# Optimization experiments

Measured on AMD Instinct MI355X. Metric: run time of the kernel, lower is better.

The kernel has to match this reference:

```python
import jax, jax.numpy as jnp
import numpy as np

N, E, C0, H, NC = 50000, 800000, 64, 64, 2500
NUM_LAYERS = 3


def setup_inputs() -> dict:
    key = jax.random.key(0)
    ks = jax.random.split(key, 16)
    inp = {}
    inp["x"] = jax.random.normal(ks[0], (N, C0), dtype=jnp.float32)
    inp["edge_index"] = jax.random.randint(ks[1], (2, E), 0, N, dtype=jnp.int64)
    inp["cluster"] = jax.random.randint(ks[2], (N,), 0, NC, dtype=jnp.int64)
    c = C0
    for i in range(NUM_LAYERS):
        inp[f"w1_{i}"] = jax.random.normal(ks[3 + 4 * i], (c, H), jnp.float32) / np.sqrt(c).astype(np.float32)
        inp[f"b1_{i}"] = jnp.zeros((H,), jnp.float32)
        inp[f"w2_{i}"] = jax.random.normal(ks[4 + 4 * i], (H, c), jnp.float32) / np.sqrt(H).astype(np.float32)
        inp[f"b2_{i}"] = jnp.zeros((c,), jnp.float32)
        c *= 2
    inp["n_clusters"] = NC
    return inp


def _glp(x, src, dst, w1, b1, w2, b2, num_nodes):
    # node encoder MLP: Linear -> ReLU -> Linear
    h = jnp.maximum(x @ w1 + b1, 0.0) @ w2 + b2  # [N, c]
    # message passing: gather at source, scatter-max at destination
    msg = h[src]  # [E, c]
    aggr = jax.ops.segment_max(msg, dst, num_segments=num_nodes)  # [N, c]
    # nodes with no incoming edges -> 0 (PyG fill for max aggregation)
    aggr = jnp.where(jnp.isfinite(aggr), aggr, 0.0)
    # update: concat(encoder_out, aggregated) -> channels double
    return jnp.concatenate([h, aggr], axis=1)


def reference(x, edge_index, cluster,
              w1_0, b1_0, w2_0, b2_0,
              w1_1, b1_1, w2_1, b2_1,
              w1_2, b1_2, w2_2, b2_2,
              n_clusters):
    num_nodes = x.shape[0]
    src, dst = edge_index[0], edge_index[1]
    params = [(w1_0, b1_0, w2_0, b2_0), (w1_1, b1_1, w2_1, b2_1), (w1_2, b1_2, w2_2, b2_2)]
    for (w1, b1, w2, b2) in params:
        x = _glp(x, src, dst, w1, b1, w2, b2, num_nodes)
    # cluster-wise max pool over polylines
    pooled = jax.ops.segment_max(x, cluster, num_segments=n_clusters)  # [NC, 512]
    pooled = jnp.where(jnp.isfinite(pooled), pooled, 0.0)
    # column-wise (dim=0) normalization as in the source
    out = pooled / (jnp.linalg.norm(pooled, axis=0) + 1e-6)
    return out
```

## Files before the change

### kernel.cpp

```cpp
#include <hip/hip_runtime.h>
#include <math.h>

typedef unsigned short bfu;
typedef __attribute__((ext_vector_type(8))) short bf16x8;
typedef __attribute__((ext_vector_type(16))) float f32x16;

__device__ __forceinline__ float b2f(bfu u) {
    unsigned int x = ((unsigned int)u) << 16;
    return __uint_as_float(x);
}
__device__ __forceinline__ bfu f2bf(float f) {
    unsigned int u = __float_as_uint(f);
    unsigned int r = (u + 0x7FFFu + ((u >> 16) & 1u)) >> 16;
    return (bfu)r;
}

struct InitArgs {
    int* deg; int N; int* cdeg; int NC; float* sumsq;
    const float* w[6]; bfu* whi[6]; bfu* wlo[6]; int K[6]; int Nw[6];
    const float* x0; bfu* xhi; bfu* xlo; int xtotal;
};

__global__ __launch_bounds__(256) void k_init(InitArgs a) {
    const int j = blockIdx.y;
    const int g0 = blockIdx.x * 256 + threadIdx.x;
    const int gs = gridDim.x * 256;
    if (j == 0) {
        for (int i = g0; i < a.N; i += gs) a.deg[i] = 0;
        for (int i = g0; i < a.NC; i += gs) a.cdeg[i] = 0;
        for (int i = g0; i < 512; i += gs) a.sumsq[i] = 0.f;
    } else if (j <= 6) {
        const int jj = j - 1;
        const int K = a.K[jj], Nw = a.Nw[jj];
        const int total = K * Nw;
        const float* w = a.w[jj];
        bfu* dhi = a.whi[jj];
        bfu* dlo = a.wlo[jj];
        for (int idx = g0; idx < total; idx += gs) {
            int k = idx / Nw, n = idx % Nw;
            float v = w[idx];
            bfu hi = f2bf(v);
            bfu lo = f2bf(v - b2f(hi));
            dhi[n * K + k] = hi;
            dlo[n * K + k] = lo;
        }
    } else {
        for (int i = g0; i * 4 < a.xtotal; i += gs) {
            int base = i * 4;
            float4 v = *(const float4*)&a.x0[base];
            ushort4 h, l;
            h.x = f2bf(v.x); l.x = f2bf(v.x - b2f(h.x));
            h.y = f2bf(v.y); l.y = f2bf(v.y - b2f(h.y));
            h.z = f2bf(v.z); l.z = f2bf(v.z - b2f(h.z));
            h.w = f2bf(v.w); l.w = f2bf(v.w - b2f(h.w));
            *(ushort4*)&a.xhi[base] = h;
            *(ushort4*)&a.xlo[base] = l;
        }
    }
}

__global__ void k_rank(const int* __restrict__ dst, int E, int* __restrict__ deg,
                       int* __restrict__ rank,
                       const int* __restrict__ cluster, int N, int* __restrict__ cdeg,
                       int* __restrict__ crank) {
    const int base = blockIdx.x * 1024 + threadIdx.x;
#pragma unroll
    for (int u = 0; u < 4; u++) {
        int e = base + u * 256;
        if (e < E) rank[e] = atomicAdd(&deg[dst[e]], 1);
    }
#pragma unroll
    for (int u = 0; u < 4; u++) {
        int i = base + u * 256;
        if (i < N) crank[i] = atomicAdd(&cdeg[cluster[i]], 1);
    }
}

__global__ __launch_bounds__(256) void k_scanA(const int* __restrict__ deg, int N,
                                               const int* __restrict__ cdeg, int NC,
                                               int* __restrict__ scn0, int* __restrict__ scn1,
                                               int* __restrict__ bsum0, int* __restrict__ bsum1) {
    __shared__ int part[256];
    const int seg = blockIdx.y;
    const int n = seg ? NC : N;
    const int* d = seg ? cdeg : deg;
    int* scn = seg ? scn1 : scn0;
    int* bs  = seg ? bsum1 : bsum0;
    const int b = blockIdx.x;
    if (b * 256 >= n) return;
    const int t = threadIdx.x;
    const int i = b * 256 + t;
    int v = (i < n) ? d[i] : 0;
    part[t] = v;
    __syncthreads();
#pragma unroll
    for (int off = 1; off < 256; off <<= 1) {
        int cv = part[t];
        int u = (t >= off) ? part[t - off] : 0;
        __syncthreads();
        part[t] = cv + u;
        __syncthreads();
    }
    if (i < n) scn[i] = part[t];
    if (t == 255) bs[b] = part[255];
}

__global__ __launch_bounds__(256) void k_scanC(const int* __restrict__ deg, int N,
                                               const int* __restrict__ cdeg, int NC,
                                               const int* __restrict__ scn0, const int* __restrict__ scn1,
                                               const int* __restrict__ bsum0, int nb0,
                                               const int* __restrict__ bsum1, int nb1,
                                               int* __restrict__ ptr0, int* __restrict__ ptr1) {
    __shared__ int part[256];
    const int seg = blockIdx.y;
    const int n = seg ? NC : N;
    const int nb = seg ? nb1 : nb0;
    const int* d = seg ? cdeg : deg;
    const int* scn = seg ? scn1 : scn0;
    const int* bsum = seg ? bsum1 : bsum0;
    int* ptr = seg ? ptr1 : ptr0;
    const int b = blockIdx.x;
    if (b * 256 >= n) return;
    const int t = threadIdx.x;
    int v = (t < nb) ? bsum[t] : 0;
    part[t] = v;
    __syncthreads();
#pragma unroll
    for (int off = 1; off < 256; off <<= 1) {
        int cv = part[t];
        int u = (t >= off) ? part[t - off] : 0;
        __syncthreads();
        part[t] = cv + u;
        __syncthreads();
    }
    const int boff = (b == 0) ? 0 : part[b - 1];
    const int i = b * 256 + t;
    if (i < n) ptr[i] = boff + scn[i] - d[i];
    if (b == 0 && t == 0) ptr[n] = part[nb - 1];
}

__global__ void k_scatter2(const int* __restrict__ dst, const int* __restrict__ src,
                           const int* __restrict__ rank, const int* __restrict__ rowptr,
                           int E, int* __restrict__ colidx,
                           const int* __restrict__ cluster, const int* __restrict__ crank,
                           const int* __restrict__ cptr, int N, int* __restrict__ cidx) {
    const int base = blockIdx.x * 1024 + threadIdx.x;
#pragma unroll
    for (int u = 0; u < 4; u++) {
        int e = base + u * 256;
        if (e < E) colidx[rowptr[dst[e]] + rank[e]] = src[e];
    }
#pragma unroll
    for (int u = 0; u < 4; u++) {
        int i = base + u * 256;
        if (i < N) cidx[cptr[cluster[i]] + crank[i]] = i;
    }
}

__device__ __forceinline__ int swz(int row, int kb) {
    return (row * 128 + (kb ^ ((row & 7) << 4))) >> 1;
}

template <bool WLO>
__global__ __launch_bounds__(256) void k_layer(const bfu* __restrict__ Ahi, const bfu* __restrict__ Alo,
                                               const bfu* __restrict__ W1hi, const bfu* __restrict__ W1lo,
                                               const float* __restrict__ b1,
                                               const bfu* __restrict__ W2hi, const bfu* __restrict__ W2lo,
                                               const float* __restrict__ b2,
                                               bfu* __restrict__ Ohi, bfu* __restrict__ Olo,
                                               int M, int K, int Kzero, int Nw2, int OS) {
    __shared__ __align__(16) bfu As[2][64 * 64];
    __shared__ __align__(16) bfu Bs[2][64 * 64];
    const int tid = threadIdx.x;
    const int wave = tid >> 6, lane = tid & 63;
    const int m0 = blockIdx.x * 64;
    const int l31 = lane & 31;
    const int khalfb = (lane >> 5) * 16;
    const int arow = (wave & 1) * 32 + l31;
    const int cbase = (wave >> 1) * 32;

    f32x16 acc;
#pragma unroll
    for (int i = 0; i < 16; i++) acc[i] = 0.f;

    for (int k0 = 0; k0 < K; k0 += 64) {
        const bool full3 = (k0 < Kzero);
#pragma unroll
        for (int i = 0; i < 2; i++) {
            int idx = i * 2048 + tid * 8;
            int row = idx >> 6;
            int ke = idx & 63;
            int gm = m0 + row; if (gm >= M) gm = M - 1;
            uint4 v = *(const uint4*)&Ahi[(size_t)gm * K + k0 + ke];
            *(uint4*)&As[0][swz(row, ke * 2)] = v;
        }
        if (full3) {
#pragma unroll
            for (int i = 0; i < 2; i++) {
                int idx = i * 2048 + tid * 8;
                int row = idx >> 6;
                int ke = idx & 63;
                int gm = m0 + row; if (gm >= M) gm = M - 1;
                uint4 v = *(const uint4*)&Alo[(size_t)gm * K + k0 + ke];
                *(uint4*)&As[1][swz(row, ke * 2)] = v;
            }
        }
#pragma unroll
        for (int p = 0; p < 2; p++) {
            const bfu* src = p ? W1lo : W1hi;
#pragma unroll
            for (int i = 0; i < 2; i++) {
                int idx = i * 2048 + tid * 8;
                int row = idx >> 6;
                int ke = idx & 63;
                uint4 v = *(const uint4*)&src[(size_t)row * K + k0 + ke];
                *(uint4*)&Bs[p][swz(row, ke * 2)] = v;
            }
        }
        __syncthreads();
#pragma unroll
        for (int s = 0; s < 4; s++) {
            int kb = s * 32 + khalfb;
            bf16x8 ah = *(const bf16x8*)&As[0][swz(arow, kb)];
            bf16x8 bh = *(const bf16x8*)&Bs[0][swz(cbase + l31, kb)];
            bf16x8 bl = *(const bf16x8*)&Bs[1][swz(cbase + l31, kb)];
            acc = __builtin_amdgcn_mfma_f32_32x32x16_bf16(ah, bh, acc, 0, 0, 0);
            acc = __builtin_amdgcn_mfma_f32_32x32x16_bf16(ah, bl, acc, 0, 0, 0);
            if (full3) {
                bf16x8 al = *(const bf16x8*)&As[1][swz(arow, kb)];
                acc = __builtin_amdgcn_mfma_f32_32x32x16_bf16(al, bh, acc, 0, 0, 0);
            }
        }
        __syncthreads();
    }

    {
        float bc = b1[cbase + l31];
        const int rbase = (wave & 1) * 32 + 4 * (lane >> 5);
#pragma unroll
        for (int r = 0; r < 16; r++) {
            int row = rbase + (r & 3) + 8 * (r >> 2);
            float t0 = fmaxf(acc[r] + bc, 0.f);
            bfu h0 = f2bf(t0);
            bfu l0 = f2bf(t0 - b2f(h0));
            As[0][swz(row, (cbase + l31) * 2)] = h0;
            As[1][swz(row, (cbase + l31) * 2)] = l0;
        }
    }

    for (int n0 = 0; n0 < Nw2; n0 += 64) {
        __syncthreads();
#pragma unroll
        for (int p = 0; p < 2; p++) {
            const bfu* src = p ? W2lo : W2hi;
#pragma unroll
            for (int i = 0; i < 2; i++) {
                int idx = i * 2048 + tid * 8;
                int row = idx >> 6;
                int ke = idx & 63;
                uint4 v = *(const uint4*)&src[(size_t)(n0 + row) * 64 + ke];
                *(uint4*)&Bs[p][swz(row, ke * 2)] = v;
            }
        }
        __syncthreads();
#pragma unroll
        for (int i = 0; i < 16; i++) acc[i] = 0.f;
#pragma unroll
        for (int s = 0; s < 4; s++) {
            int kb = s * 32 + khalfb;
            bf16x8 th = *(const bf16x8*)&As[0][swz(arow, kb)];
            bf16x8 tl = *(const bf16x8*)&As[1][swz(arow, kb)];
            bf16x8 wh = *(const bf16x8*)&Bs[0][swz(cbase + l31, kb)];
            bf16x8 wl = *(const bf16x8*)&Bs[1][swz(cbase + l31, kb)];
            acc = __builtin_amdgcn_mfma_f32_32x32x16_bf16(th, wh, acc, 0, 0, 0);
            acc = __builtin_amdgcn_mfma_f32_32x32x16_bf16(th, wl, acc, 0, 0, 0);
            acc = __builtin_amdgcn_mfma_f32_32x32x16_bf16(tl, wh, acc, 0, 0, 0);
        }
        float bc = b2[n0 + cbase + l31];
        const int rbase = m0 + (wave & 1) * 32 + 4 * (lane >> 5);
#pragma unroll
        for (int r = 0; r < 16; r++) {
            int grow = rbase + (r & 3) + 8 * (r >> 2);
            if (grow < M) {
                float o0 = acc[r] + bc;
                bfu h0 = f2bf(o0);
                size_t base = (size_t)grow * OS + n0 + cbase;
                Ohi[base + l31] = h0;
                if (WLO) {
                    Olo[base + l31] = f2bf(o0 - b2f(h0));
                }
            }
        }
    }
}

template <int R>
__device__ __forceinline__ void gmax(const bfu* __restrict__ p, float* acc) {
    if (R == 4) {
        ushort4 v = *(const ushort4*)p;
        acc[0] = fmaxf(acc[0], b2f(v.x)); acc[1] = fmaxf(acc[1], b2f(v.y));
        acc[2] = fmaxf(acc[2], b2f(v.z)); acc[3] = fmaxf(acc[3], b2f(v.w));
    } else if (R == 2) {
        ushort2 v = *(const ushort2*)p;
        acc[0] = fmaxf(acc[0], b2f(v.x)); acc[1] = fmaxf(acc[1], b2f(v.y));
    } else {
        acc[0] = fmaxf(acc[0], b2f(*p));
    }
}

template <int R>
__global__ void k_agg(const bfu* __restrict__ hplane, bfu* __restrict__ whi,
                      const int* __restrict__ rowptr, const int* __restrict__ colidx,
                      int N, int stride) {
    const int wid = (blockIdx.x * blockDim.x + threadIdx.x) >> 6;
    const int lane = threadIdx.x & 63;
    if (wid >= N) return;
    const int beg = rowptr[wid], end = rowptr[wid + 1];
    const int ch = lane * R;

    float acc[R];
#pragma unroll
    for (int r = 0; r < R; r++) acc[r] = -INFINITY;

    int i = beg;
    for (; i + 8 <= end; i += 8) {
        int off[8];
#pragma unroll
        for (int u = 0; u < 8; u++) off[u] = colidx[i + u] * stride + ch;
#pragma unroll
        for (int u = 0; u < 8; u++) gmax<R>(hplane + off[u], acc);
    }
    for (; i + 2 <= end; i += 2) {
        int o0 = colidx[i] * stride + ch;
        int o1 = colidx[i + 1] * stride + ch;
        gmax<R>(hplane + o0, acc);
        gmax<R>(hplane + o1, acc);
    }
    if (i < end) gmax<R>(hplane + colidx[i] * stride + ch, acc);

    if (beg == end) {
#pragma unroll
        for (int r = 0; r < R; r++) acc[r] = 0.f;
    }
    int obase = wid * stride + 64 * R + ch;
#pragma unroll
    for (int r = 0; r < R; r++) whi[obase + r] = f2bf(acc[r]);
}

__global__ void k_pool(const bfu* __restrict__ xhi,
                       const int* __restrict__ cptr, const int* __restrict__ cidx,
                       float* __restrict__ pooled) {
    int cl = blockIdx.x;
    int tid = threadIdx.x;
    int beg = cptr[cl], end = cptr[cl + 1];
    float ax = -INFINITY, ay = -INFINITY;
    int i = beg;
    for (; i + 4 <= end; i += 4) {
        ushort2 h0 = *(const ushort2*)&xhi[cidx[i + 0] * 512 + tid * 2];
        ushort2 h1 = *(const ushort2*)&xhi[cidx[i + 1] * 512 + tid * 2];
        ushort2 h2 = *(const ushort2*)&xhi[cidx[i + 2] * 512 + tid * 2];
        ushort2 h3 = *(const ushort2*)&xhi[cidx[i + 3] * 512 + tid * 2];
        ax = fmaxf(ax, fmaxf(fmaxf(b2f(h0.x), b2f(h1.x)), fmaxf(b2f(h2.x), b2f(h3.x))));
        ay = fmaxf(ay, fmaxf(fmaxf(b2f(h0.y), b2f(h1.y)), fmaxf(b2f(h2.y), b2f(h3.y))));
    }
    for (; i < end; i++) {
        ushort2 h = *(const ushort2*)&xhi[cidx[i] * 512 + tid * 2];
        ax = fmaxf(ax, b2f(h.x)); ay = fmaxf(ay, b2f(h.y));
    }
    if (beg == end) { ax = 0.f; ay = 0.f; }
    float2 o; o.x = ax; o.y = ay;
    *(float2*)&pooled[(size_t)cl * 512 + tid * 2] = o;
}

__global__ void k_sumsq(const float* __restrict__ pooled, float* __restrict__ sumsq, int NC) {
    int tid = threadIdx.x;
    float ax = 0.f, ay = 0.f;
    for (int r = blockIdx.x; r < NC; r += gridDim.x) {
        float2 v = *(const float2*)&pooled[(size_t)r * 512 + tid * 2];
        ax += v.x * v.x; ay += v.y * v.y;
    }
    atomicAdd(&sumsq[tid * 2 + 0], ax);
    atomicAdd(&sumsq[tid * 2 + 1], ay);
}

__global__ void k_scale(const float* __restrict__ pooled, const float* __restrict__ sumsq,
                        float* __restrict__ out, int total) {
    int i = blockIdx.x * blockDim.x + threadIdx.x;
    int base = i * 4;
    if (base < total) {
        float4 v = *(const float4*)&pooled[base];
        int col = base & 511;
        v.x /= (sqrtf(sumsq[col + 0]) + 1e-6f);
        v.y /= (sqrtf(sumsq[col + 1]) + 1e-6f);
        v.z /= (sqrtf(sumsq[col + 2]) + 1e-6f);
        v.w /= (sqrtf(sumsq[col + 3]) + 1e-6f);
        *(float4*)&out[base] = v;
    }
}

extern "C" void kernel_launch(void* const* d_in, const int* in_sizes, int n_in,
                              void* d_out, int out_size, void* d_ws, size_t ws_size,
                              hipStream_t stream) {
    const float* x0      = (const float*)d_in[0];
    const int*   ei      = (const int*)d_in[1];
    const int*   cluster = (const int*)d_in[2];
    const float* w1_[3] = {(const float*)d_in[3], (const float*)d_in[7],  (const float*)d_in[11]};
    const float* b1_[3] = {(const float*)d_in[4], (const float*)d_in[8],  (const float*)d_in[12]};
    const float* w2_[3] = {(const float*)d_in[5], (const float*)d_in[9],  (const float*)d_in[13]};
    const float* b2_[3] = {(const float*)d_in[6], (const float*)d_in[10], (const float*)d_in[14]};

    const int N  = in_sizes[2];
    const int E  = in_sizes[1] / 2;
    const int NC = 2500;
    float* out = (float*)d_out;

    char* p = (char*)d_ws;
    auto alloc = [&](size_t bytes) -> char* {
        char* r = p;
        p += (bytes + 255) & ~(size_t)255;
        return r;
    };
    bfu* X0hi = (bfu*)alloc((size_t)N * 64 * 2);
    bfu* X0lo = (bfu*)alloc((size_t)N * 64 * 2);
    bfu* X1hi = (bfu*)alloc((size_t)N * 128 * 2);
    bfu* X1lo = (bfu*)alloc((size_t)N * 128 * 2);
    bfu* X2hi = (bfu*)alloc((size_t)N * 256 * 2);
    bfu* X2lo = (bfu*)alloc((size_t)N * 256 * 2);
    bfu* X3hi = (bfu*)alloc((size_t)N * 512 * 2);
    bfu* w1t_hi[3]; bfu* w1t_lo[3]; bfu* w2t_hi[3]; bfu* w2t_lo[3];
    const int Ks[3] = {64, 128, 256};
    for (int l = 0; l < 3; l++) {
        w1t_hi[l] = (bfu*)alloc((size_t)64 * Ks[l] * 2);
        w1t_lo[l] = (bfu*)alloc((size_t)64 * Ks[l] * 2);
        w2t_hi[l] = (bfu*)alloc((size_t)Ks[l] * 64 * 2);
        w2t_lo[l] = (bfu*)alloc((size_t)Ks[l] * 64 * 2);
    }
    float* pooled = (float*)alloc((size_t)NC * 512 * 4);
    float* sumsq  = (float*)alloc(512 * 4);
    int*   deg    = (int*)alloc((size_t)(N + 1) * 4);
    int*   rowptr = (int*)alloc((size_t)(N + 1) * 4);
    int*   rank   = (int*)alloc((size_t)E * 4);
    int*   colidx = (int*)alloc((size_t)E * 4);
    int*   cdeg   = (int*)alloc((size_t)(NC + 1) * 4);
    int*   cptr   = (int*)alloc((size_t)(NC + 1) * 4);
    int*   crank  = (int*)alloc((size_t)N * 4);
    int*   cidx   = (int*)alloc((size_t)N * 4);
    int*   scn0   = (int*)alloc((size_t)N * 4);
    int*   scn1   = (int*)alloc((size_t)NC * 4);
    int*   bsum0  = (int*)alloc(256 * 4);
    int*   bsum1  = (int*)alloc(256 * 4);

    const int* src = ei;
    const int* dst = ei + E;

    InitArgs ia;
    ia.deg = deg; ia.N = N; ia.cdeg = cdeg; ia.NC = NC; ia.sumsq = sumsq;
    for (int l = 0; l < 3; l++) {
        ia.w[2 * l]     = w1_[l]; ia.whi[2 * l]     = w1t_hi[l]; ia.wlo[2 * l]     = w1t_lo[l];
        ia.K[2 * l]     = Ks[l];  ia.Nw[2 * l]      = 64;
        ia.w[2 * l + 1] = w2_[l]; ia.whi[2 * l + 1] = w2t_hi[l]; ia.wlo[2 * l + 1] = w2t_lo[l];
        ia.K[2 * l + 1] = 64;     ia.Nw[2 * l + 1]  = Ks[l];
    }
    ia.x0 = x0; ia.xhi = X0hi; ia.xlo = X0lo; ia.xtotal = N * 64;
    k_init<<<dim3(128, 8), 256, 0, stream>>>(ia);

    k_rank<<<(E + 1023) / 1024, 256, 0, stream>>>(dst, E, deg, rank, cluster, N, cdeg, crank);

    const int nb0 = (N + 255) / 256;
    const int nb1 = (NC + 255) / 256;
    k_scanA<<<dim3(nb0, 2), 256, 0, stream>>>(deg, N, cdeg, NC, scn0, scn1, bsum0, bsum1);
    k_scanC<<<dim3(nb0, 2), 256, 0, stream>>>(deg, N, cdeg, NC, scn0, scn1, bsum0, nb0, bsum1, nb1,
                                              rowptr, cptr);

    k_scatter2<<<(E + 1023) / 1024, 256, 0, stream>>>(dst, src, rank, rowptr, E, colidx,
                                                      cluster, crank, cptr, N, cidx);

    const int Mt = (N + 63) / 64;
    const int aggBlocks = (N * 64 + 255) / 256;

    k_layer<true><<<Mt, 256, 0, stream>>>(X0hi, X0lo, w1t_hi[0], w1t_lo[0], b1_[0],
                                          w2t_hi[0], w2t_lo[0], b2_[0], X1hi, X1lo,
                                          N, 64, 64, 64, 128);
    k_agg<1><<<aggBlocks, 256, 0, stream>>>(X1hi, X1hi, rowptr, colidx, N, 128);

    k_layer<true><<<Mt, 256, 0, stream>>>(X1hi, X1lo, w1t_hi[1], w1t_lo[1], b1_[1],
                                          w2t_hi[1], w2t_lo[1], b2_[1], X2hi, X2lo,
                                          N, 128, 64, 128, 256);
    k_agg<2><<<aggBlocks, 256, 0, stream>>>(X2hi, X2hi, rowptr, colidx, N, 256);

    k_layer<false><<<Mt, 256, 0, stream>>>(X2hi, X2lo, w1t_hi[2], w1t_lo[2], b1_[2],
                                           w2t_hi[2], w2t_lo[2], b2_[2], X3hi, nullptr,
                                           N, 256, 128, 256, 512);
    k_agg<4><<<aggBlocks, 256, 0, stream>>>(X3hi, X3hi, rowptr, colidx, N, 512);

    k_pool<<<NC, 256, 0, stream>>>(X3hi, cptr, cidx, pooled);
    k_sumsq<<<64, 256, 0, stream>>>(pooled, sumsq, NC);
    k_scale<<<(out_size / 4 + 255) / 256, 256, 0, stream>>>(pooled, sumsq, out, out_size);
}
```

Measured before the change: 277.3 us.

## Fuse CSR build and post-pool stages into cooperative kernels with grid syncs

Measured after the change: 735.5 us. +165.3%, slower.

```diff
diff --git a/kernel.cpp b/kernel.cpp
--- a/kernel.cpp
+++ b/kernel.cpp
@@ -1,5 +1,8 @@
 #include <hip/hip_runtime.h>
+#include <hip/hip_cooperative_groups.h>
 #include <math.h>
+
+namespace cg = cooperative_groups;
 
 typedef unsigned short bfu;
 typedef __attribute__((ext_vector_type(8))) short bf16x8;
@@ -59,101 +62,99 @@
     }
 }
 
-__global__ void k_rank(const int* __restrict__ dst, int E, int* __restrict__ deg,
-                       int* __restrict__ rank,
-                       const int* __restrict__ cluster, int N, int* __restrict__ cdeg,
-                       int* __restrict__ crank) {
-    const int base = blockIdx.x * 1024 + threadIdx.x;
-#pragma unroll
-    for (int u = 0; u < 4; u++) {
-        int e = base + u * 256;
-        if (e < E) rank[e] = atomicAdd(&deg[dst[e]], 1);
-    }
-#pragma unroll
-    for (int u = 0; u < 4; u++) {
-        int i = base + u * 256;
-        if (i < N) crank[i] = atomicAdd(&cdeg[cluster[i]], 1);
-    }
-}
-
-__global__ __launch_bounds__(256) void k_scanA(const int* __restrict__ deg, int N,
-                                               const int* __restrict__ cdeg, int NC,
-                                               int* __restrict__ scn0, int* __restrict__ scn1,
-                                               int* __restrict__ bsum0, int* __restrict__ bsum1) {
+__global__ __launch_bounds__(256) void k_csr(const int* __restrict__ dst, const int* __restrict__ src,
+                                             int E, const int* __restrict__ cluster, int N, int NC,
+                                             int* __restrict__ deg, int* __restrict__ cdeg,
+                                             int* __restrict__ rank, int* __restrict__ crank,
+                                             int* __restrict__ scn0, int* __restrict__ scn1,
+                                             int* __restrict__ bsum0, int* __restrict__ bsum1,
+                                             int* __restrict__ rowptr, int* __restrict__ cptr,
+                                             int* __restrict__ colidx, int* __restrict__ cidx,
+                                             int nb0, int nb1) {
+    cg::grid_group grid = cg::this_grid();
     __shared__ int part[256];
-    const int seg = blockIdx.y;
-    const int n = seg ? NC : N;
-    const int* d = seg ? cdeg : deg;
-    int* scn = seg ? scn1 : scn0;
-    int* bs  = seg ? bsum1 : bsum0;
+    const int tid = threadIdx.x;
     const int b = blockIdx.x;
-    if (b * 256 >= n) return;
-    const int t = threadIdx.x;
-    const int i = b * 256 + t;
-    int v = (i < n) ? d[i] : 0;
-    part[t] = v;
-    __syncthreads();
-#pragma unroll
-    for (int off = 1; off < 256; off <<= 1) {
-        int cv = part[t];
-        int u = (t >= off) ? part[t - off] : 0;
-        __syncthreads();
-        part[t] = cv + u;
-        __syncthreads();
-    }
-    if (i < n) scn[i] = part[t];
-    if (t == 255) bs[b] = part[255];
-}
-
-__global__ __launch_bounds__(256) void k_scanC(const int* __restrict__ deg, int N,
-                                               const int* __restrict__ cdeg, int NC,
-                                               const int* __restrict__ scn0, const int* __restrict__ scn1,
-                                               const int* __restrict__ bsum0, int nb0,
-                                               const int* __restrict__ bsum1, int nb1,
-                                               int* __restrict__ ptr0, int* __restrict__ ptr1) {
-    __shared__ int part[256];
-    const int seg = blockIdx.y;
-    const int n = seg ? NC : N;
-    const int nb = seg ? nb1 : nb0;
-    const int* d = seg ? cdeg : deg;
-    const int* scn = seg ? scn1 : scn0;
-    const int* bsum = seg ? bsum1 : bsum0;
-    int* ptr = seg ? ptr1 : ptr0;
-    const int b = blockIdx.x;
-    if (b * 256 >= n) return;
-    const int t = threadIdx.x;
-    int v = (t < nb) ? bsum[t] : 0;
-    part[t] = v;
-    __syncthreads();
-#pragma unroll
-    for (int off = 1; off < 256; off <<= 1) {
-        int cv = part[t];
-        int u = (t >= off) ? part[t - off] : 0;
-        __syncthreads();
-        part[t] = cv + u;
-        __syncthreads();
-    }
-    const int boff = (b == 0) ? 0 : part[b - 1];
-    const int i = b * 256 + t;
-    if (i < n) ptr[i] = boff + scn[i] - d[i];
-    if (b == 0 && t == 0) ptr[n] = part[nb - 1];
-}
-
-__global__ void k_scatter2(const int* __restrict__ dst, const int* __restrict__ src,
-                           const int* __restrict__ rank, const int* __restrict__ rowptr,
-                           int E, int* __restrict__ colidx,
-                           const int* __restrict__ cluster, const int* __restrict__ crank,
-                           const int* __restrict__ cptr, int N, int* __restrict__ cidx) {
-    const int base = blockIdx.x * 1024 + threadIdx.x;
-#pragma unroll
-    for (int u = 0; u < 4; u++) {
-        int e = base + u * 256;
-        if (e < E) colidx[rowptr[dst[e]] + rank[e]] = src[e];
-    }
-#pragma unroll
-    for (int u = 0; u < 4; u++) {
-        int i = base + u * 256;
-        if (i < N) cidx[cptr[cluster[i]] + crank[i]] = i;
+
+    {
+        const int base = b * 1024 + tid;
+#pragma unroll
+        for (int u = 0; u < 4; u++) {
+            int e = base + u * 256;
+            if (e < E) rank[e] = atomicAdd(&deg[dst[e]], 1);
+        }
+#pragma unroll
+        for (int u = 0; u < 4; u++) {
+            int i = base + u * 256;
+            if (i < N) crank[i] = atomicAdd(&cdeg[cluster[i]], 1);
+        }
+    }
+    grid.sync();
+
+    if (b < nb0 + nb1) {
+        const int seg = (b >= nb0);
+        const int n = seg ? NC : N;
+        const int* d = seg ? cdeg : deg;
+        int* scn = seg ? scn1 : scn0;
+        int* bs  = seg ? bsum1 : bsum0;
+        const int bb = seg ? (b - nb0) : b;
+        const int i = bb * 256 + tid;
+        int v = (i < n) ? d[i] : 0;
+        part[tid] = v;
+        __syncthreads();
+#pragma unroll
+        for (int off = 1; off < 256; off <<= 1) {
+            int cv = part[tid];
+            int u = (tid >= off) ? part[tid - off] : 0;
+            __syncthreads();
+            part[tid] = cv + u;
+            __syncthreads();
+        }
+        if (i < n) scn[i] = part[tid];
+        if (tid == 255) bs[bb] = part[255];
+    }
+    grid.sync();
+
+    if (b < nb0 + nb1) {
+        const int seg = (b >= nb0);
+        const int n = seg ? NC : N;
+        const int nb = seg ? nb1 : nb0;
+        const int* d = seg ? cdeg : deg;
+        const int* scn = seg ? scn1 : scn0;
+        const int* bsum = seg ? bsum1 : bsum0;
+        int* ptr = seg ? cptr : rowptr;
+        const int bb = seg ? (b - nb0) : b;
+        int v = (tid < nb) ? bsum[tid] : 0;
+        __syncthreads();
+        part[tid] = v;
+        __syncthreads();
+#pragma unroll
+        for (int off = 1; off < 256; off <<= 1) {
+            int cv = part[tid];
+            int u = (tid >= off) ? part[tid - off] : 0;
+            __syncthreads();
+            part[tid] = cv + u;
+            __syncthreads();
+        }
+        const int boff = (bb == 0) ? 0 : part[bb - 1];
+        const int i = bb * 256 + tid;
+        if (i < n) ptr[i] = boff + scn[i] - d[i];
+        if (bb == 0 && tid == 0) ptr[n] = part[nb - 1];
+    }
+    grid.sync();
+
+    {
+        const int base = b * 1024 + tid;
+#pragma unroll
+        for (int u = 0; u < 4; u++) {
+            int e = base + u * 256;
+            if (e < E) colidx[rowptr[dst[e]] + rank[e]] = src[e];
+        }
+#pragma unroll
+        for (int u = 0; u < 4; u++) {
+            int i = base + u * 256;
+            if (i < N) cidx[cptr[cluster[i]] + crank[i]] = i;
+        }
     }
 }
 
@@ -347,47 +348,48 @@
     for (int r = 0; r < R; r++) whi[obase + r] = f2bf(acc[r]);
 }
 
-__global__ void k_pool(const bfu* __restrict__ xhi,
-                       const int* __restrict__ cptr, const int* __restrict__ cidx,
-                       float* __restrict__ pooled) {
-    int cl = blockIdx.x;
-    int tid = threadIdx.x;
-    int beg = cptr[cl], end = cptr[cl + 1];
-    float ax = -INFINITY, ay = -INFINITY;
-    int i = beg;
-    for (; i + 4 <= end; i += 4) {
-        ushort2 h0 = *(const ushort2*)&xhi[cidx[i + 0] * 512 + tid * 2];
-        ushort2 h1 = *(const ushort2*)&xhi[cidx[i + 1] * 512 + tid * 2];
-        ushort2 h2 = *(const ushort2*)&xhi[cidx[i + 2] * 512 + tid * 2];
-        ushort2 h3 = *(const ushort2*)&xhi[cidx[i + 3] * 512 + tid * 2];
-        ax = fmaxf(ax, fmaxf(fmaxf(b2f(h0.x), b2f(h1.x)), fmaxf(b2f(h2.x), b2f(h3.x))));
-        ay = fmaxf(ay, fmaxf(fmaxf(b2f(h0.y), b2f(h1.y)), fmaxf(b2f(h2.y), b2f(h3.y))));
-    }
-    for (; i < end; i++) {
-        ushort2 h = *(const ushort2*)&xhi[cidx[i] * 512 + tid * 2];
-        ax = fmaxf(ax, b2f(h.x)); ay = fmaxf(ay, b2f(h.y));
-    }
-    if (beg == end) { ax = 0.f; ay = 0.f; }
-    float2 o; o.x = ax; o.y = ay;
-    *(float2*)&pooled[(size_t)cl * 512 + tid * 2] = o;
-}
-
-__global__ void k_sumsq(const float* __restrict__ pooled, float* __restrict__ sumsq, int NC) {
-    int tid = threadIdx.x;
-    float ax = 0.f, ay = 0.f;
-    for (int r = blockIdx.x; r < NC; r += gridDim.x) {
-        float2 v = *(const float2*)&pooled[(size_t)r * 512 + tid * 2];
-        ax += v.x * v.x; ay += v.y * v.y;
-    }
-    atomicAdd(&sumsq[tid * 2 + 0], ax);
-    atomicAdd(&sumsq[tid * 2 + 1], ay);
-}
-
-__global__ void k_scale(const float* __restrict__ pooled, const float* __restrict__ sumsq,
-                        float* __restrict__ out, int total) {
-    int i = blockIdx.x * blockDim.x + threadIdx.x;
-    int base = i * 4;
-    if (base < total) {
+__global__ __launch_bounds__(256) void k_post(const bfu* __restrict__ xhi,
+                                              const int* __restrict__ cptr, const int* __restrict__ cidx,
+                                              float* __restrict__ pooled, float* __restrict__ sumsq,
+                                              float* __restrict__ out, int NC, int total) {
+    cg::grid_group grid = cg::this_grid();
+    const int tid = threadIdx.x;
+
+    for (int cl = blockIdx.x; cl < NC; cl += gridDim.x) {
+        int beg = cptr[cl], end = cptr[cl + 1];
+        float ax = -INFINITY, ay = -INFINITY;
+        int i = beg;
+        for (; i + 4 <= end; i += 4) {
+            ushort2 h0 = *(const ushort2*)&xhi[cidx[i + 0] * 512 + tid * 2];
+            ushort2 h1 = *(const ushort2*)&xhi[cidx[i + 1] * 512 + tid * 2];
+            ushort2 h2 = *(const ushort2*)&xhi[cidx[i + 2] * 512 + tid * 2];
+            ushort2 h3 = *(const ushort2*)&xhi[cidx[i + 3] * 512 + tid * 2];
+            ax = fmaxf(ax, fmaxf(fmaxf(b2f(h0.x), b2f(h1.x)), fmaxf(b2f(h2.x), b2f(h3.x))));
+            ay = fmaxf(ay, fmaxf(fmaxf(b2f(h0.y), b2f(h1.y)), fmaxf(b2f(h2.y), b2f(h3.y))));
+        }
+        for (; i < end; i++) {
+            ushort2 h = *(const ushort2*)&xhi[cidx[i] * 512 + tid * 2];
+            ax = fmaxf(ax, b2f(h.x)); ay = fmaxf(ay, b2f(h.y));
+        }
+        if (beg == end) { ax = 0.f; ay = 0.f; }
+        float2 o; o.x = ax; o.y = ay;
+        *(float2*)&pooled[(size_t)cl * 512 + tid * 2] = o;
+    }
+    grid.sync();
+
+    if (blockIdx.x < 64) {
+        float ax = 0.f, ay = 0.f;
+        for (int r = blockIdx.x; r < NC; r += 64) {
+            float2 v = *(const float2*)&pooled[(size_t)r * 512 + tid * 2];
+            ax += v.x * v.x; ay += v.y * v.y;
+        }
+        atomicAdd(&sumsq[tid * 2 + 0], ax);
+        atomicAdd(&sumsq[tid * 2 + 1], ay);
+    }
+    grid.sync();
+
+    for (int i = blockIdx.x * 256 + tid; i * 4 < total; i += gridDim.x * 256) {
+        int base = i * 4;
         float4 v = *(const float4*)&pooled[base];
         int col = base & 511;
         v.x /= (sqrtf(sumsq[col + 0]) + 1e-6f);
@@ -450,8 +452,8 @@
     int*   bsum0  = (int*)alloc(256 * 4);
     int*   bsum1  = (int*)alloc(256 * 4);
 
-    const int* src = ei;
-    const int* dst = ei + E;
+    const int* srcp = ei;
+    const int* dstp = ei + E;
 
     InitArgs ia;
     ia.deg = deg; ia.N = N; ia.cdeg = cdeg; ia.NC = NC; ia.sumsq = sumsq;
@@ -464,16 +466,19 @@
     ia.x0 = x0; ia.xhi = X0hi; ia.xlo = X0lo; ia.xtotal = N * 64;
     k_init<<<dim3(128, 8), 256, 0, stream>>>(ia);
 
-    k_rank<<<(E + 1023) / 1024, 256, 0, stream>>>(dst, E, deg, rank, cluster, N, cdeg, crank);
-
-    const int nb0 = (N + 255) / 256;
-    const int nb1 = (NC + 255) / 256;
-    k_scanA<<<dim3(nb0, 2), 256, 0, stream>>>(deg, N, cdeg, NC, scn0, scn1, bsum0, bsum1);
-    k_scanC<<<dim3(nb0, 2), 256, 0, stream>>>(deg, N, cdeg, NC, scn0, scn1, bsum0, nb0, bsum1, nb1,
-                                              rowptr, cptr);
-
-    k_scatter2<<<(E + 1023) / 1024, 256, 0, stream>>>(dst, src, rank, rowptr, E, colidx,
-                                                      cluster, crank, cptr, N, cidx);
+    int nb0 = (N + 255) / 256;
+    int nb1 = (NC + 255) / 256;
+    int csrBlocks = (E + 1023) / 1024;
+    if (csrBlocks < nb0 + nb1) csrBlocks = nb0 + nb1;
+    {
+        void* args[] = {(void*)&dstp, (void*)&srcp, (void*)&E, (void*)&cluster,
+                        (void*)&N, (void*)&NC,
+                        (void*)&deg, (void*)&cdeg, (void*)&rank, (void*)&crank,
+                        (void*)&scn0, (void*)&scn1, (void*)&bsum0, (void*)&bsum1,
+                        (void*)&rowptr, (void*)&cptr, (void*)&colidx, (void*)&cidx,
+                        (void*)&nb0, (void*)&nb1};
+        hipLaunchCooperativeKernel((void*)k_csr, dim3(csrBlocks), dim3(256), args, 0, stream);
+    }
 
     const int Mt = (N + 63) / 64;
     const int aggBlocks = (N * 64 + 255) / 256;
@@ -493,7 +498,11 @@
                                            N, 256, 128, 256, 512);
     k_agg<4><<<aggBlocks, 256, 0, stream>>>(X3hi, X3hi, rowptr, colidx, N, 512);
 
-    k_pool<<<NC, 256, 0, stream>>>(X3hi, cptr, cidx, pooled);
-    k_sumsq<<<64, 256, 0, stream>>>(pooled, sumsq, NC);
-    k_scale<<<(out_size / 4 + 255) / 256, 256, 0, stream>>>(pooled, sumsq, out, out_size);
-}
+    {
+        int total = out_size;
+        void* args[] = {(void*)&X3hi, (void*)&cptr, (void*)&cidx,
+                        (void*)&pooled, (void*)&sumsq, (void*)&out,
+                        (void*)&NC, (void*)&total};
+        hipLaunchCooperativeKernel((void*)k_post, dim3(1024), dim3(256), args, 0, stream);
+    }
+}
```

## Fuse neighbor max-aggregation into next layer's GEMM A-tile load

Applied to the files above, without the earlier changes.

New measurement: 353.4 us. 1.27x slower.

```diff
diff --git a/kernel.cpp b/kernel.cpp
--- a/kernel.cpp
+++ b/kernel.cpp
@@ -161,13 +161,14 @@
     return (row * 128 + (kb ^ ((row & 7) << 4))) >> 1;
 }
 
-template <bool WLO>
+template <int AGGR, bool WLO>
 __global__ __launch_bounds__(256) void k_layer(const bfu* __restrict__ Ahi, const bfu* __restrict__ Alo,
                                                const bfu* __restrict__ W1hi, const bfu* __restrict__ W1lo,
                                                const float* __restrict__ b1,
                                                const bfu* __restrict__ W2hi, const bfu* __restrict__ W2lo,
                                                const float* __restrict__ b2,
                                                bfu* __restrict__ Ohi, bfu* __restrict__ Olo,
+                                               const int* __restrict__ rowptr, const int* __restrict__ colidx,
                                                int M, int K, int Kzero, int Nw2, int OS) {
     __shared__ __align__(16) bfu As[2][64 * 64];
     __shared__ __align__(16) bfu Bs[2][64 * 64];
@@ -185,15 +186,6 @@
 
     for (int k0 = 0; k0 < K; k0 += 64) {
         const bool full3 = (k0 < Kzero);
-#pragma unroll
-        for (int i = 0; i < 2; i++) {
-            int idx = i * 2048 + tid * 8;
-            int row = idx >> 6;
-            int ke = idx & 63;
-            int gm = m0 + row; if (gm >= M) gm = M - 1;
-            uint4 v = *(const uint4*)&Ahi[(size_t)gm * K + k0 + ke];
-            *(uint4*)&As[0][swz(row, ke * 2)] = v;
-        }
         if (full3) {
 #pragma unroll
             for (int i = 0; i < 2; i++) {
@@ -201,8 +193,47 @@
                 int row = idx >> 6;
                 int ke = idx & 63;
                 int gm = m0 + row; if (gm >= M) gm = M - 1;
-                uint4 v = *(const uint4*)&Alo[(size_t)gm * K + k0 + ke];
+                uint4 v = *(const uint4*)&Ahi[(size_t)gm * Kzero + k0 + ke];
+                *(uint4*)&As[0][swz(row, ke * 2)] = v;
+            }
+#pragma unroll
+            for (int i = 0; i < 2; i++) {
+                int idx = i * 2048 + tid * 8;
+                int row = idx >> 6;
+                int ke = idx & 63;
+                int gm = m0 + row; if (gm >= M) gm = M - 1;
+                uint4 v = *(const uint4*)&Alo[(size_t)gm * Kzero + k0 + ke];
                 *(uint4*)&As[1][swz(row, ke * 2)] = v;
+            }
+        } else if (AGGR > 0) {
+            const int koff = k0 - Kzero;
+            const int ch = koff + lane;
+            for (int r = 0; r < 16; r++) {
+                int row = wave * 16 + r;
+                int gnode = m0 + row;
+                float ag = 0.f;
+                if (gnode < M) {
+                    int beg = rowptr[gnode], end = rowptr[gnode + 1];
+                    if (beg < end) {
+                        ag = -INFINITY;
+                        int i = beg;
+                        for (; i + 8 <= end; i += 8) {
+                            int off[8];
+#pragma unroll
+                            for (int u = 0; u < 8; u++) off[u] = colidx[i + u] * Kzero + ch;
+#pragma unroll
+                            for (int u = 0; u < 8; u++) ag = fmaxf(ag, b2f(Ahi[off[u]]));
+                        }
+                        for (; i + 2 <= end; i += 2) {
+                            int o0 = colidx[i] * Kzero + ch;
+                            int o1 = colidx[i + 1] * Kzero + ch;
+                            ag = fmaxf(ag, b2f(Ahi[o0]));
+                            ag = fmaxf(ag, b2f(Ahi[o1]));
+                        }
+                        if (i < end) ag = fmaxf(ag, b2f(Ahi[colidx[i] * Kzero + ch]));
+                    }
+                }
+                As[0][swz(row, lane * 2)] = f2bf(ag);
             }
         }
 #pragma unroll
@@ -422,10 +453,10 @@
     };
     bfu* X0hi = (bfu*)alloc((size_t)N * 64 * 2);
     bfu* X0lo = (bfu*)alloc((size_t)N * 64 * 2);
-    bfu* X1hi = (bfu*)alloc((size_t)N * 128 * 2);
-    bfu* X1lo = (bfu*)alloc((size_t)N * 128 * 2);
-    bfu* X2hi = (bfu*)alloc((size_t)N * 256 * 2);
-    bfu* X2lo = (bfu*)alloc((size_t)N * 256 * 2);
+    bfu* X1hi = (bfu*)alloc((size_t)N * 64 * 2);
+    bfu* X1lo = (bfu*)alloc((size_t)N * 64 * 2);
+    bfu* X2hi = (bfu*)alloc((size_t)N * 128 * 2);
+    bfu* X2lo = (bfu*)alloc((size_t)N * 128 * 2);
     bfu* X3hi = (bfu*)alloc((size_t)N * 512 * 2);
     bfu* w1t_hi[3]; bfu* w1t_lo[3]; bfu* w2t_hi[3]; bfu* w2t_lo[3];
     const int Ks[3] = {64, 128, 256};
@@ -478,19 +509,18 @@
     const int Mt = (N + 63) / 64;
     const int aggBlocks = (N * 64 + 255) / 256;
 
-    k_layer<true><<<Mt, 256, 0, stream>>>(X0hi, X0lo, w1t_hi[0], w1t_lo[0], b1_[0],
-                                          w2t_hi[0], w2t_lo[0], b2_[0], X1hi, X1lo,
-                                          N, 64, 64, 64, 128);
-    k_agg<1><<<aggBlocks, 256, 0, stream>>>(X1hi, X1hi, rowptr, colidx, N, 128);
-
-    k_layer<true><<<Mt, 256, 0, stream>>>(X1hi, X1lo, w1t_hi[1], w1t_lo[1], b1_[1],
-                                          w2t_hi[1], w2t_lo[1], b2_[1], X2hi, X2lo,
-                                          N, 128, 64, 128, 256);
-    k_agg<2><<<aggBlocks, 256, 0, stream>>>(X2hi, X2hi, rowptr, colidx, N, 256);
-
-    k_layer<false><<<Mt, 256, 0, stream>>>(X2hi, X2lo, w1t_hi[2], w1t_lo[2], b1_[2],
-                                           w2t_hi[2], w2t_lo[2], b2_[2], X3hi, nullptr,
-                                           N, 256, 128, 256, 512);
+    k_layer<0, true><<<Mt, 256, 0, stream>>>(X0hi, X0lo, w1t_hi[0], w1t_lo[0], b1_[0],
+                                             w2t_hi[0], w2t_lo[0], b2_[0], X1hi, X1lo,
+                                             nullptr, nullptr, N, 64, 64, 64, 64);
+
+    k_layer<1, true><<<Mt, 256, 0, stream>>>(X1hi, X1lo, w1t_hi[1], w1t_lo[1], b1_[1],
+                                             w2t_hi[1], w2t_lo[1], b2_[1], X2hi, X2lo,
+                                             rowptr, colidx, N, 128, 64, 128, 128);
+
+    k_layer<2, false><<<Mt, 256, 0, stream>>>(X2hi, X2lo, w1t_hi[2], w1t_lo[2], b1_[2],
+                                              w2t_hi[2], w2t_lo[2], b2_[2], X3hi, nullptr,
+                                              rowptr, colidx, N, 256, 128, 256, 512);
+
     k_agg<4><<<aggBlocks, 256, 0, stream>>>(X3hi, X3hi, rowptr, colidx, N, 512);
 
     k_pool<<<NC, 256, 0, stream>>>(X3hi, cptr, cidx, pooled);
```
